# Kernel tuning notes

Hardware: AMD Instinct MI355X
Metric: run time of the kernel (lower is better)

Reference implementation:

```python
import jax, jax.numpy as jnp
import numpy as np

MAX_ITER = 10
EPS = 1e-4


def setup_inputs() -> dict:
    key = jax.random.key(0)
    k1, k2, k3 = jax.random.split(key, 3)
    B, N, M = 64, 1024, 1024
    s = jax.random.uniform(k1, (B, N, M), dtype=jnp.float32)
    nrows = jax.random.randint(k2, (B,), 0, N, dtype=jnp.int64 if jax.config.read('jax_enable_x64') else jnp.int32)
    ncols = jax.random.randint(k3, (B,), 0, M, dtype=nrows.dtype)
    return {"s": s, "nrows": nrows, "ncols": ncols}


def _sinkhorn(s, nrows, ncols):
    # Faithful to torch Sinkhorn.forward with exp=False, dummy_row=False.
    # The torch code builds [B,N,N]/[B,M,M] block-of-ones matrices and matmuls;
    # mathematically this is a masked column-sum (even iters) / row-sum (odd iters)
    # over the valid nrows[b] x ncols[b] block, followed by division inside the
    # block and zeroing outside it.
    B, N, M = s.shape
    row_mask = jnp.arange(N)[None, :] < nrows[:, None]            # [B, N]
    col_mask = jnp.arange(M)[None, :] < ncols[:, None]            # [B, M]
    mask = row_mask[:, :, None] & col_mask[:, None, :]            # [B, N, M]

    out = s + EPS
    for i in range(MAX_ITER):
        if i % 2 == 0:
            # column sums over valid rows -> [B, 1, M]
            sm = jnp.sum(jnp.where(row_mask[:, :, None], out, 0.0), axis=1, keepdims=True)
        else:
            # row sums over valid cols -> [B, N, 1]
            sm = jnp.sum(jnp.where(col_mask[:, None, :], out, 0.0), axis=2, keepdims=True)
        sm = jnp.where(sm == 0, 1.0, sm)  # guard (only affects masked-out entries)
        out = jnp.where(mask, out / sm, 0.0)
    return out


def reference(s, nrows, ncols):
    return _sinkhorn(s, nrows, ncols)
```

## Files before the change

### kernel.cpp

```cpp
#include <hip/hip_runtime.h>
#include <hip/hip_fp16.h>

#define EPS 1e-4f
constexpr int N_DIM  = 1024;
constexpr int M_DIM  = 1024;
constexpr int BATCH  = 64;
constexpr int CH     = 16;
constexpr int NPHASE = 5;


__global__ void zero_cnt(unsigned int* cnt) {
    const int t = threadIdx.x;
    if (t < NPHASE * BATCH) cnt[t] = 0u;
}

__device__ __forceinline__ void bat_barrier(unsigned int* cnt, int idx,
                                            unsigned int nact) {
    __syncthreads();
    if (threadIdx.x == 0) {
        __threadfence();
        atomicAdd(&cnt[idx], 1u);
        while (__hip_atomic_load(&cnt[idx], __ATOMIC_ACQUIRE,
                                 __HIP_MEMORY_SCOPE_AGENT) < nact)
            __builtin_amdgcn_s_sleep(8);
    }
    __syncthreads();
    __threadfence();
}

__global__ __launch_bounds__(256, 4)
void sinkhorn_one(const float* __restrict__ s,
                  const int* __restrict__ nrows,
                  const int* __restrict__ ncols,
                  __half* __restrict__ h,
                  float* __restrict__ tp0,
                  float* __restrict__ tp1,
                  unsigned int* __restrict__ cnt,
                  float* __restrict__ out)
{
    const int b  = blockIdx.y;
    const int ch = blockIdx.x;
    const int R = nrows[b], C = ncols[b];
    const size_t base = (size_t)b * N_DIM * M_DIM;
    const int tid = threadIdx.x, lane = tid & 63, wv = tid >> 6;
    const float4 z4 = make_float4(0.f, 0.f, 0.f, 0.f);

    for (int n = R + ch; n < N_DIM; n += CH)
        *(float4*)(out + base + (size_t)n * M_DIM + tid * 4) = z4;

    if (R == 0) return;
    const int CR = (R + CH - 1) / CH;
    const unsigned int nact = (unsigned int)((R + CR - 1) / CR);
    if ((unsigned int)ch >= nact) return;
    const int n0 = ch * CR;
    const int rows = min(R - n0, CR);
    const bool hi = (C > 512);

    __shared__ float clds[M_DIM];
    __shared__ float tp_lds[4][M_DIM];

    {
        const int m = tid * 4;
        float4 acc = z4;
        if (m < C) {
            for (int nn = 0; nn < rows; ++nn) {
                const size_t off = base + (size_t)(n0 + nn) * M_DIM + m;
                float4 v = *(const float4*)(s + off);
                v.x += EPS;
                v.y = (m + 1 < C) ? v.y + EPS : 0.f;
                v.z = (m + 2 < C) ? v.z + EPS : 0.f;
                v.w = (m + 3 < C) ? v.w + EPS : 0.f;
                acc.x += v.x; acc.y += v.y; acc.z += v.z; acc.w += v.w;
                union { __half2 h2[2]; uint2 u2; } pk;
                pk.h2[0] = __floats2half2_rn(v.x, v.y);
                pk.h2[1] = __floats2half2_rn(v.z, v.w);
                *(uint2*)(h + off) = pk.u2;
            }
        } else if (m < 512 || hi) {
            const uint2 zz = make_uint2(0u, 0u);
            for (int nn = 0; nn < rows; ++nn)
                *(uint2*)(h + base + (size_t)(n0 + nn) * M_DIM + m) = zz;
        }
        *(float4*)(tp0 + (size_t)(ch * BATCH + b) * M_DIM + m) = acc;
    }
    bat_barrier(cnt, 0 * BATCH + b, nact);

    const float* tpIn  = tp0;
    float*       tpOut = tp1;
    float crlo[8], crhi[8];

    for (int step = 0; step < 4; ++step) {
        {
            const int m = tid * 4;
            if (m < 512 || hi) {
                float4 sum = z4;
                for (unsigned int cc = 0; cc < nact; ++cc) {
                    float4 p = *(const float4*)(tpIn + (size_t)(cc * BATCH + b) * M_DIM + m);
                    sum.x += p.x; sum.y += p.y; sum.z += p.z; sum.w += p.w;
                }
                float4 cv;
                cv.x = (sum.x == 0.f) ? 1.f : 1.f / sum.x;
                cv.y = (sum.y == 0.f) ? 1.f : 1.f / sum.y;
                cv.z = (sum.z == 0.f) ? 1.f : 1.f / sum.z;
                cv.w = (sum.w == 0.f) ? 1.f : 1.f / sum.w;
                *(float4*)&clds[m] = cv;
            }
        }
        __syncthreads();
        {
            float4 a  = *(const float4*)&clds[lane * 8];
            float4 bb = *(const float4*)&clds[lane * 8 + 4];
            crlo[0]=a.x; crlo[1]=a.y; crlo[2]=a.z; crlo[3]=a.w;
            crlo[4]=bb.x; crlo[5]=bb.y; crlo[6]=bb.z; crlo[7]=bb.w;
            if (hi) {
                float4 d = *(const float4*)&clds[512 + lane * 8];
                float4 e = *(const float4*)&clds[512 + lane * 8 + 4];
                crhi[0]=d.x; crhi[1]=d.y; crhi[2]=d.z; crhi[3]=d.w;
                crhi[4]=e.x; crhi[5]=e.y; crhi[6]=e.z; crhi[7]=e.w;
            }
        }

        float tplo[8] = {0,0,0,0,0,0,0,0};
        float tphi[8] = {0,0,0,0,0,0,0,0};

        for (int nn = wv; nn < rows; nn += 4) {
            const int n = n0 + nn;
            const __half* hrow = h + base + (size_t)n * M_DIM;
            uint4 rlo = *(const uint4*)(hrow + lane * 8);
            float flo[8], fhi[8];
            {
                const __half2* hp = (const __half2*)&rlo;
#pragma unroll
                for (int k = 0; k < 4; ++k) {
                    float2 f = __half22float2(hp[k]);
                    flo[2*k] = f.x; flo[2*k+1] = f.y;
                }
            }
            float dot = 0.f;
#pragma unroll
            for (int k = 0; k < 8; ++k) dot += flo[k] * crlo[k];
            if (hi) {
                uint4 rhi = *(const uint4*)(hrow + 512 + lane * 8);
                const __half2* hq = (const __half2*)&rhi;
#pragma unroll
                for (int k = 0; k < 4; ++k) {
                    float2 f = __half22float2(hq[k]);
                    fhi[2*k] = f.x; fhi[2*k+1] = f.y;
                }
#pragma unroll
                for (int k = 0; k < 8; ++k) dot += fhi[k] * crhi[k];
            }
#pragma unroll
            for (int off = 32; off; off >>= 1) dot += __shfl_xor(dot, off);
            const float r = (dot == 0.f) ? 1.f : 1.f / dot;
#pragma unroll
            for (int k = 0; k < 8; ++k) tplo[k] += flo[k] * r;
            if (hi) {
#pragma unroll
                for (int k = 0; k < 8; ++k) tphi[k] += fhi[k] * r;
            }
        }

#pragma unroll
        for (int k = 0; k < 8; ++k) tp_lds[wv][lane * 8 + k] = tplo[k];
        if (hi) {
#pragma unroll
            for (int k = 0; k < 8; ++k) tp_lds[wv][512 + lane * 8 + k] = tphi[k];
        }
        __syncthreads();
        {
            const int m = tid * 4;
            if (m < 512 || hi) {
                float4 s0 = *(const float4*)&tp_lds[0][m];
                float4 s1 = *(const float4*)&tp_lds[1][m];
                float4 s2 = *(const float4*)&tp_lds[2][m];
                float4 s3 = *(const float4*)&tp_lds[3][m];
                *(float4*)(tpOut + (size_t)(ch * BATCH + b) * M_DIM + m) =
                    make_float4(s0.x+s1.x+s2.x+s3.x, s0.y+s1.y+s2.y+s3.y,
                                s0.z+s1.z+s2.z+s3.z, s0.w+s1.w+s2.w+s3.w);
            }
        }
        bat_barrier(cnt, (1 + step) * BATCH + b, nact);
        const float* ti = tpOut; tpOut = (float*)tpIn; tpIn = ti;
    }

    {
        const int m = tid * 4;
        if (m < 512 || hi) {
            float4 sum = z4;
            for (unsigned int cc = 0; cc < nact; ++cc) {
                float4 p = *(const float4*)(tpIn + (size_t)(cc * BATCH + b) * M_DIM + m);
                sum.x += p.x; sum.y += p.y; sum.z += p.z; sum.w += p.w;
            }
            float4 cv;
            cv.x = (sum.x == 0.f) ? 1.f : 1.f / sum.x;
            cv.y = (sum.y == 0.f) ? 1.f : 1.f / sum.y;
            cv.z = (sum.z == 0.f) ? 1.f : 1.f / sum.z;
            cv.w = (sum.w == 0.f) ? 1.f : 1.f / sum.w;
            *(float4*)&clds[m] = cv;
        }
    }
    __syncthreads();
    {
        float4 a  = *(const float4*)&clds[lane * 8];
        float4 bb = *(const float4*)&clds[lane * 8 + 4];
        crlo[0]=a.x; crlo[1]=a.y; crlo[2]=a.z; crlo[3]=a.w;
        crlo[4]=bb.x; crlo[5]=bb.y; crlo[6]=bb.z; crlo[7]=bb.w;
        if (hi) {
            float4 d = *(const float4*)&clds[512 + lane * 8];
            float4 e = *(const float4*)&clds[512 + lane * 8 + 4];
            crhi[0]=d.x; crhi[1]=d.y; crhi[2]=d.z; crhi[3]=d.w;
            crhi[4]=e.x; crhi[5]=e.y; crhi[6]=e.z; crhi[7]=e.w;
        }
    }
    for (int nn = wv; nn < rows; nn += 4) {
        const int n = n0 + nn;
        float* orow = out + base + (size_t)n * M_DIM;
        const __half* hrow = h + base + (size_t)n * M_DIM;
        uint4 rlo = *(const uint4*)(hrow + lane * 8);
        float flo[8], fhi[8];
        {
            const __half2* hp = (const __half2*)&rlo;
#pragma unroll
            for (int k = 0; k < 4; ++k) {
                float2 f = __half22float2(hp[k]);
                flo[2*k] = f.x; flo[2*k+1] = f.y;
            }
        }
        float dot = 0.f;
#pragma unroll
        for (int k = 0; k < 8; ++k) dot += flo[k] * crlo[k];
        if (hi) {
            uint4 rhi = *(const uint4*)(hrow + 512 + lane * 8);
            const __half2* hq = (const __half2*)&rhi;
#pragma unroll
            for (int k = 0; k < 4; ++k) {
                float2 f = __half22float2(hq[k]);
                fhi[2*k] = f.x; fhi[2*k+1] = f.y;
            }
#pragma unroll
            for (int k = 0; k < 8; ++k) dot += fhi[k] * crhi[k];
        }
#pragma unroll
        for (int off = 32; off; off >>= 1) dot += __shfl_xor(dot, off);
        const float r = (dot == 0.f) ? 1.f : 1.f / dot;

        *(float4*)(orow + lane * 8)     = make_float4(flo[0]*r*crlo[0], flo[1]*r*crlo[1],
                                                      flo[2]*r*crlo[2], flo[3]*r*crlo[3]);
        *(float4*)(orow + lane * 8 + 4) = make_float4(flo[4]*r*crlo[4], flo[5]*r*crlo[5],
                                                      flo[6]*r*crlo[6], flo[7]*r*crlo[7]);
        float4 o2 = z4, o3 = z4;
        if (hi) {
            o2 = make_float4(fhi[0]*r*crhi[0], fhi[1]*r*crhi[1],
                             fhi[2]*r*crhi[2], fhi[3]*r*crhi[3]);
            o3 = make_float4(fhi[4]*r*crhi[4], fhi[5]*r*crhi[5],
                             fhi[6]*r*crhi[6], fhi[7]*r*crhi[7]);
        }
        *(float4*)(orow + 512 + lane * 8)     = o2;
        *(float4*)(orow + 512 + lane * 8 + 4) = o3;
    }
}

constexpr int FCROWS = N_DIM / CH;

__global__ __launch_bounds__(256)
void conv_col0(const float* __restrict__ s, const int* __restrict__ nrows,
               const int* __restrict__ ncols, __half* __restrict__ h,
               float* __restrict__ tp0) {
    const int b  = blockIdx.y;
    const int mt = blockIdx.x & 3;
    const int ch = blockIdx.x >> 2;
    const int R = nrows[b], C = ncols[b];
    const int n0 = ch * FCROWS;
    if (n0 >= R) return;
    const int lane = threadIdx.x & 63, wv = threadIdx.x >> 6;
    const int m = mt * 256 + lane * 4;
    const int nend = min(R, n0 + FCROWS);
    const size_t base = (size_t)b * N_DIM * M_DIM;

    float4 acc = make_float4(0.f, 0.f, 0.f, 0.f);
    if (mt * 256 < C) {
        for (int n = n0 + wv; n < nend; n += 4) {
            float4 v = *(const float4*)(s + base + (size_t)n * M_DIM + m);
            v.x = (m + 0 < C) ? v.x + EPS : 0.f;
            v.y = (m + 1 < C) ? v.y + EPS : 0.f;
            v.z = (m + 2 < C) ? v.z + EPS : 0.f;
            v.w = (m + 3 < C) ? v.w + EPS : 0.f;
            acc.x += v.x; acc.y += v.y; acc.z += v.z; acc.w += v.w;
            union { __half2 h2[2]; uint2 u2; } pk;
            pk.h2[0] = __floats2half2_rn(v.x, v.y);
            pk.h2[1] = __floats2half2_rn(v.z, v.w);
            *(uint2*)(h + base + (size_t)n * M_DIM + m) = pk.u2;
        }
    } else {
        const uint2 z = make_uint2(0u, 0u);
        for (int n = n0 + wv; n < nend; n += 4)
            *(uint2*)(h + base + (size_t)n * M_DIM + m) = z;
    }
    __shared__ float4 red[4][64];
    red[wv][lane] = acc;
    __syncthreads();
    if (wv == 0) {
        float4 a0 = red[0][lane], a1 = red[1][lane],
               a2 = red[2][lane], a3 = red[3][lane];
        *(float4*)(tp0 + (size_t)(ch * BATCH + b) * M_DIM + m) =
            make_float4(a0.x+a1.x+a2.x+a3.x, a0.y+a1.y+a2.y+a3.y,
                        a0.z+a1.z+a2.z+a3.z, a0.w+a1.w+a2.w+a3.w);
    }
}

template <bool FINAL>
__global__ __launch_bounds__(256)
void row_step(const __half* __restrict__ h, const int* __restrict__ nrows,
              const int* __restrict__ ncols, const float* __restrict__ tpIn,
              float* __restrict__ tpOut, float* __restrict__ out) {
    const int b  = blockIdx.y;
    const int ch = blockIdx.x;
    const int R = nrows[b], C = ncols[b];
    const int n0 = ch * FCROWS;
    if (!FINAL && n0 >= R) return;
    const int lane = threadIdx.x & 63, wv = threadIdx.x >> 6;
    const size_t base = (size_t)b * N_DIM * M_DIM;
    const bool hi = (C > 512);
    const bool anyrows = (n0 < R);

    __shared__ float clds[M_DIM];
    __shared__ float tp_lds[4][M_DIM];

    float crlo[8], crhi[8];
    if (anyrows) {
        const int nch = min(CH, (R + FCROWS - 1) / FCROWS);
        const int t4 = threadIdx.x * 4;
        if (hi || t4 < 512) {
            float4 sum = make_float4(0.f, 0.f, 0.f, 0.f);
            for (int cc = 0; cc < nch; ++cc) {
                float4 p = *(const float4*)(tpIn + (size_t)(cc * BATCH + b) * M_DIM + t4);
                sum.x += p.x; sum.y += p.y; sum.z += p.z; sum.w += p.w;
            }
            float4 cv;
            cv.x = (sum.x == 0.f) ? 1.f : 1.f / sum.x;
            cv.y = (sum.y == 0.f) ? 1.f : 1.f / sum.y;
            cv.z = (sum.z == 0.f) ? 1.f : 1.f / sum.z;
            cv.w = (sum.w == 0.f) ? 1.f : 1.f / sum.w;
            *(float4*)&clds[t4] = cv;
        }
        __syncthreads();
        float4 a = *(const float4*)&clds[lane * 8];
        float4 bb = *(const float4*)&clds[lane * 8 + 4];
        crlo[0]=a.x; crlo[1]=a.y; crlo[2]=a.z; crlo[3]=a.w;
        crlo[4]=bb.x; crlo[5]=bb.y; crlo[6]=bb.z; crlo[7]=bb.w;
        if (hi) {
            float4 d = *(const float4*)&clds[512 + lane * 8];
            float4 e = *(const float4*)&clds[512 + lane * 8 + 4];
            crhi[0]=d.x; crhi[1]=d.y; crhi[2]=d.z; crhi[3]=d.w;
            crhi[4]=e.x; crhi[5]=e.y; crhi[6]=e.z; crhi[7]=e.w;
        }
    }

    float tplo[8] = {0,0,0,0,0,0,0,0};
    float tphi[8] = {0,0,0,0,0,0,0,0};

    for (int i = 0; i < 16; ++i) {
        const int n = n0 + wv * 16 + i;
        if (n < R) {
            const __half* hrow = h + base + (size_t)n * M_DIM;
            uint4 rlo = *(const uint4*)(hrow + lane * 8);
            float flo[8], fhi[8];
            const __half2* hp = (const __half2*)&rlo;
#pragma unroll
            for (int k = 0; k < 4; ++k) {
                float2 f = __half22float2(hp[k]);
                flo[2*k] = f.x; flo[2*k+1] = f.y;
            }
            float dot = 0.f;
#pragma unroll
            for (int k = 0; k < 8; ++k) dot += flo[k] * crlo[k];
            if (hi) {
                uint4 rhi = *(const uint4*)(hrow + 512 + lane * 8);
                const __half2* hq = (const __half2*)&rhi;
#pragma unroll
                for (int k = 0; k < 4; ++k) {
                    float2 f = __half22float2(hq[k]);
                    fhi[2*k] = f.x; fhi[2*k+1] = f.y;
                }
#pragma unroll
                for (int k = 0; k < 8; ++k) dot += fhi[k] * crhi[k];
            }
#pragma unroll
            for (int off = 32; off; off >>= 1) dot += __shfl_xor(dot, off);
            const float r = (dot == 0.f) ? 1.f : 1.f / dot;

            if (FINAL) {
                float* orow = out + base + (size_t)n * M_DIM;
                *(float4*)(orow + lane * 8)     = make_float4(flo[0]*r*crlo[0], flo[1]*r*crlo[1],
                                                              flo[2]*r*crlo[2], flo[3]*r*crlo[3]);
                *(float4*)(orow + lane * 8 + 4) = make_float4(flo[4]*r*crlo[4], flo[5]*r*crlo[5],
                                                              flo[6]*r*crlo[6], flo[7]*r*crlo[7]);
                float4 o2 = make_float4(0.f,0.f,0.f,0.f), o3 = o2;
                if (hi) {
                    o2 = make_float4(fhi[0]*r*crhi[0], fhi[1]*r*crhi[1],
                                     fhi[2]*r*crhi[2], fhi[3]*r*crhi[3]);
                    o3 = make_float4(fhi[4]*r*crhi[4], fhi[5]*r*crhi[5],
                                     fhi[6]*r*crhi[6], fhi[7]*r*crhi[7]);
                }
                *(float4*)(orow + 512 + lane * 8)     = o2;
                *(float4*)(orow + 512 + lane * 8 + 4) = o3;
            } else {
#pragma unroll
                for (int k = 0; k < 8; ++k) tplo[k] += flo[k] * r;
                if (hi) {
#pragma unroll
                    for (int k = 0; k < 8; ++k) tphi[k] += fhi[k] * r;
                }
            }
        } else if (FINAL) {
            float* orow = out + base + (size_t)n * M_DIM;
            const float4 z = make_float4(0.f, 0.f, 0.f, 0.f);
            *(float4*)(orow + lane * 8)           = z;
            *(float4*)(orow + lane * 8 + 4)       = z;
            *(float4*)(orow + 512 + lane * 8)     = z;
            *(float4*)(orow + 512 + lane * 8 + 4) = z;
        }
    }

    if (!FINAL) {
#pragma unroll
        for (int k = 0; k < 8; ++k) tp_lds[wv][lane * 8 + k] = tplo[k];
        if (hi) {
#pragma unroll
            for (int k = 0; k < 8; ++k) tp_lds[wv][512 + lane * 8 + k] = tphi[k];
        }
        __syncthreads();
        const int t4 = threadIdx.x * 4;
        if (hi || t4 < 512) {
            float4 s0 = *(const float4*)&tp_lds[0][t4];
            float4 s1 = *(const float4*)&tp_lds[1][t4];
            float4 s2 = *(const float4*)&tp_lds[2][t4];
            float4 s3 = *(const float4*)&tp_lds[3][t4];
            *(float4*)(tpOut + (size_t)(ch * BATCH + b) * M_DIM + t4) =
                make_float4(s0.x+s1.x+s2.x+s3.x, s0.y+s1.y+s2.y+s3.y,
                            s0.z+s1.z+s2.z+s3.z, s0.w+s1.w+s2.w+s3.w);
        }
    }
}

extern "C" void kernel_launch(void* const* d_in, const int* in_sizes, int n_in,
                              void* d_out, int out_size, void* d_ws, size_t ws_size,
                              hipStream_t stream) {
    const float* s     = (const float*)d_in[0];
    const int*   nrows = (const int*)d_in[1];
    const int*   ncols = (const int*)d_in[2];
    float*       out   = (float*)d_out;

    const size_t hElems  = (size_t)BATCH * N_DIM * M_DIM;
    const size_t tpElems = (size_t)CH * BATCH * M_DIM;
    const size_t need    = hElems * 2 + 2 * tpElems * 4 + NPHASE * BATCH * 4;

    if (ws_size >= need) {
        __half* h   = (__half*)d_ws;
        float*  tp0 = (float*)(h + hElems);
        float*  tp1 = tp0 + tpElems;
        unsigned int* cnt = (unsigned int*)(tp1 + tpElems);

        int dev = 0, numCU = 0, perCU = 0;
        hipGetDevice(&dev);
        hipDeviceGetAttribute(&numCU, hipDeviceAttributeMultiprocessorCount, dev);
        hipOccupancyMaxActiveBlocksPerMultiprocessor(&perCU, sinkhorn_one, 256, 0);

        if ((long long)perCU * numCU >= CH * BATCH) {
            zero_cnt<<<1, 320, 0, stream>>>(cnt);
            void* args[] = {(void*)&s, (void*)&nrows, (void*)&ncols, (void*)&h,
                            (void*)&tp0, (void*)&tp1, (void*)&cnt, (void*)&out};
            hipLaunchCooperativeKernel((void*)sinkhorn_one, dim3(CH, BATCH),
                                       dim3(256), args, 0, stream);
            return;
        }

        dim3 convGrid(4 * CH, BATCH), kGrid(CH, BATCH);
        conv_col0<<<convGrid, 256, 0, stream>>>(s, nrows, ncols, h, tp0);
        row_step<false><<<kGrid, 256, 0, stream>>>(h, nrows, ncols, tp0, tp1, out);
        row_step<false><<<kGrid, 256, 0, stream>>>(h, nrows, ncols, tp1, tp0, out);
        row_step<false><<<kGrid, 256, 0, stream>>>(h, nrows, ncols, tp0, tp1, out);
        row_step<false><<<kGrid, 256, 0, stream>>>(h, nrows, ncols, tp1, tp0, out);
        row_step<true ><<<kGrid, 256, 0, stream>>>(h, nrows, ncols, tp0, tp1, out);
        return;
    }
}
```

Measured before the change: 210.7 us.

## Distribute blocks across batches proportionally to valid rows; store partial sums as fp16

```diff
diff --git a/kernel.cpp b/kernel.cpp
--- a/kernel.cpp
+++ b/kernel.cpp
@@ -5,8 +5,10 @@
 constexpr int N_DIM  = 1024;
 constexpr int M_DIM  = 1024;
 constexpr int BATCH  = 64;
+constexpr int NB     = 1024;
+constexpr int NPHASE = 5;
+constexpr int WPAD   = 256;
 constexpr int CH     = 16;
-constexpr int NPHASE = 5;
 
 
 __global__ void zero_cnt(unsigned int* cnt) {
@@ -28,33 +30,63 @@
     __threadfence();
 }
 
+__device__ __forceinline__ void tp_store(__half* tp, size_t idx, float4 v) {
+    union { __half2 h2[2]; uint2 u; } pk;
+    pk.h2[0] = __floats2half2_rn(v.x, v.y);
+    pk.h2[1] = __floats2half2_rn(v.z, v.w);
+    *(uint2*)(tp + idx) = pk.u;
+}
+
 __global__ __launch_bounds__(256, 4)
-void sinkhorn_one(const float* __restrict__ s,
-                  const int* __restrict__ nrows,
-                  const int* __restrict__ ncols,
-                  __half* __restrict__ h,
-                  float* __restrict__ tp0,
-                  float* __restrict__ tp1,
-                  unsigned int* __restrict__ cnt,
-                  float* __restrict__ out)
+void sinkhorn_prop(const float* __restrict__ s,
+                   const int* __restrict__ nrows,
+                   const int* __restrict__ ncols,
+                   __half* __restrict__ h,
+                   __half* __restrict__ tp0,
+                   __half* __restrict__ tp1,
+                   unsigned int* __restrict__ cnt,
+                   float* __restrict__ out)
 {
-    const int b  = blockIdx.y;
-    const int ch = blockIdx.x;
-    const int R = nrows[b], C = ncols[b];
+    const int tid = threadIdx.x, lane = tid & 63, wv = tid >> 6;
+    __shared__ int sR[BATCH];
+    __shared__ int sNb[BATCH];
+    __shared__ int sPfx[BATCH + 1];
+
+    if (tid < BATCH) sR[tid] = nrows[tid];
+    __syncthreads();
+    if (tid == 0) {
+        long tot = 0;
+        for (int i = 0; i < BATCH; ++i) tot += sR[i] + WPAD;
+        int acc = 0;
+        for (int i = 0; i < BATCH; ++i) {
+            int nb = 1 + (int)(((long)(NB - BATCH) * (sR[i] + WPAD)) / tot);
+            sNb[i] = nb; sPfx[i] = acc; acc += nb;
+        }
+        sPfx[BATCH] = acc;
+    }
+    __syncthreads();
+
+    const int g = blockIdx.x;
+    if (g >= sPfx[BATCH]) return;
+    int b = BATCH - 1;
+    for (int i = 0; i < BATCH; ++i) { if (g < sPfx[i + 1]) { b = i; break; } }
+    const int l   = g - sPfx[b];
+    const int nbb = sNb[b];
+    const int R = sR[b], C = ncols[b];
     const size_t base = (size_t)b * N_DIM * M_DIM;
-    const int tid = threadIdx.x, lane = tid & 63, wv = tid >> 6;
     const float4 z4 = make_float4(0.f, 0.f, 0.f, 0.f);
 
-    for (int n = R + ch; n < N_DIM; n += CH)
+    for (int n = R + l; n < N_DIM; n += nbb)
         *(float4*)(out + base + (size_t)n * M_DIM + tid * 4) = z4;
-
     if (R == 0) return;
-    const int CR = (R + CH - 1) / CH;
+
+    const int CR = (R + nbb - 1) / nbb;
     const unsigned int nact = (unsigned int)((R + CR - 1) / CR);
-    if ((unsigned int)ch >= nact) return;
-    const int n0 = ch * CR;
+    if ((unsigned int)l >= nact) return;
+    const int n0 = l * CR;
     const int rows = min(R - n0, CR);
     const bool hi = (C > 512);
+    const int g0 = sPfx[b];
 
     __shared__ float clds[M_DIM];
     __shared__ float tp_lds[4][M_DIM];
@@ -81,12 +113,13 @@
             for (int nn = 0; nn < rows; ++nn)
                 *(uint2*)(h + base + (size_t)(n0 + nn) * M_DIM + m) = zz;
         }
-        *(float4*)(tp0 + (size_t)(ch * BATCH + b) * M_DIM + m) = acc;
+        if (m < 512 || hi)
+            tp_store(tp0, (size_t)g * M_DIM + m, acc);
     }
     bat_barrier(cnt, 0 * BATCH + b, nact);
 
-    const float* tpIn  = tp0;
-    float*       tpOut = tp1;
+    const __half* tpIn  = tp0;
+    __half*       tpOut = tp1;
     float crlo[8], crhi[8];
 
     for (int step = 0; step < 4; ++step) {
@@ -95,8 +128,11 @@
             if (m < 512 || hi) {
                 float4 sum = z4;
                 for (unsigned int cc = 0; cc < nact; ++cc) {
-                    float4 p = *(const float4*)(tpIn + (size_t)(cc * BATCH + b) * M_DIM + m);
-                    sum.x += p.x; sum.y += p.y; sum.z += p.z; sum.w += p.w;
+                    uint2 raw = *(const uint2*)(tpIn + (size_t)(g0 + cc) * M_DIM + m);
+                    const __half2* hp = (const __half2*)&raw;
+                    float2 f0 = __half22float2(hp[0]);
+                    float2 f1 = __half22float2(hp[1]);
+                    sum.x += f0.x; sum.y += f0.y; sum.z += f1.x; sum.w += f1.y;
                 }
                 float4 cv;
                 cv.x = (sum.x == 0.f) ? 1.f : 1.f / sum.x;
@@ -124,8 +160,7 @@
         float tphi[8] = {0,0,0,0,0,0,0,0};
 
         for (int nn = wv; nn < rows; nn += 4) {
-            const int n = n0 + nn;
-            const __half* hrow = h + base + (size_t)n * M_DIM;
+            const __half* hrow = h + base + (size_t)(n0 + nn) * M_DIM;
             uint4 rlo = *(const uint4*)(hrow + lane * 8);
             float flo[8], fhi[8];
             {
@@ -175,13 +210,13 @@
                 float4 s1 = *(const float4*)&tp_lds[1][m];
                 float4 s2 = *(const float4*)&tp_lds[2][m];
                 float4 s3 = *(const float4*)&tp_lds[3][m];
-                *(float4*)(tpOut + (size_t)(ch * BATCH + b) * M_DIM + m) =
-                    make_float4(s0.x+s1.x+s2.x+s3.x, s0.y+s1.y+s2.y+s3.y,
-                                s0.z+s1.z+s2.z+s3.z, s0.w+s1.w+s2.w+s3.w);
+                tp_store(tpOut, (size_t)g * M_DIM + m,
+                         make_float4(s0.x+s1.x+s2.x+s3.x, s0.y+s1.y+s2.y+s3.y,
+                                     s0.z+s1.z+s2.z+s3.z, s0.w+s1.w+s2.w+s3.w));
             }
         }
         bat_barrier(cnt, (1 + step) * BATCH + b, nact);
-        const float* ti = tpOut; tpOut = (float*)tpIn; tpIn = ti;
+        const __half* ti = tpOut; tpOut = (__half*)tpIn; tpIn = ti;
     }
 
     {
@@ -189,8 +224,11 @@
         if (m < 512 || hi) {
             float4 sum = z4;
             for (unsigned int cc = 0; cc < nact; ++cc) {
-                float4 p = *(const float4*)(tpIn + (size_t)(cc * BATCH + b) * M_DIM + m);
-                sum.x += p.x; sum.y += p.y; sum.z += p.z; sum.w += p.w;
+                uint2 raw = *(const uint2*)(tpIn + (size_t)(g0 + cc) * M_DIM + m);
+                const __half2* hp = (const __half2*)&raw;
+                float2 f0 = __half22float2(hp[0]);
+                float2 f1 = __half22float2(hp[1]);
+                sum.x += f0.x; sum.y += f0.y; sum.z += f1.x; sum.w += f1.y;
             }
             float4 cv;
             cv.x = (sum.x == 0.f) ? 1.f : 1.f / sum.x;
@@ -213,6 +251,7 @@
             crhi[4]=e.x; crhi[5]=e.y; crhi[6]=e.z; crhi[7]=e.w;
         }
     }
+    const float4 z0 = make_float4(0.f, 0.f, 0.f, 0.f);
     for (int nn = wv; nn < rows; nn += 4) {
         const int n = n0 + nn;
         float* orow = out + base + (size_t)n * M_DIM;
@@ -249,7 +288,7 @@
                                                       flo[2]*r*crlo[2], flo[3]*r*crlo[3]);
         *(float4*)(orow + lane * 8 + 4) = make_float4(flo[4]*r*crlo[4], flo[5]*r*crlo[5],
                                                       flo[6]*r*crlo[6], flo[7]*r*crlo[7]);
-        float4 o2 = z4, o3 = z4;
+        float4 o2 = z0, o3 = z0;
         if (hi) {
             o2 = make_float4(fhi[0]*r*crhi[0], fhi[1]*r*crhi[1],
                              fhi[2]*r*crhi[2], fhi[3]*r*crhi[3]);
@@ -452,37 +491,40 @@
     const int*   ncols = (const int*)d_in[2];
     float*       out   = (float*)d_out;
 
-    const size_t hElems  = (size_t)BATCH * N_DIM * M_DIM;
-    const size_t tpElems = (size_t)CH * BATCH * M_DIM;
-    const size_t need    = hElems * 2 + 2 * tpElems * 4 + NPHASE * BATCH * 4;
+    const size_t hElems   = (size_t)BATCH * N_DIM * M_DIM;
+    const size_t tpRegion = (size_t)16 * 1024 * 1024;
+    const size_t need     = hElems * 2 + tpRegion + NPHASE * BATCH * 4;
 
     if (ws_size >= need) {
-        __half* h   = (__half*)d_ws;
-        float*  tp0 = (float*)(h + hElems);
-        float*  tp1 = tp0 + tpElems;
-        unsigned int* cnt = (unsigned int*)(tp1 + tpElems);
+        __half* h    = (__half*)d_ws;
+        char*   tpRg = (char*)(h + hElems);
+        unsigned int* cnt = (unsigned int*)(tpRg + tpRegion);
 
         int dev = 0, numCU = 0, perCU = 0;
         hipGetDevice(&dev);
         hipDeviceGetAttribute(&numCU, hipDeviceAttributeMultiprocessorCount, dev);
-        hipOccupancyMaxActiveBlocksPerMultiprocessor(&perCU, sinkhorn_one, 256, 0);
-
-        if ((long long)perCU * numCU >= CH * BATCH) {
+        hipOccupancyMaxActiveBlocksPerMultiprocessor(&perCU, sinkhorn_prop, 256, 0);
+
+        if ((long long)perCU * numCU >= NB) {
+            __half* tp0 = (__half*)tpRg;
+            __half* tp1 = tp0 + (size_t)NB * M_DIM;
             zero_cnt<<<1, 320, 0, stream>>>(cnt);
             void* args[] = {(void*)&s, (void*)&nrows, (void*)&ncols, (void*)&h,
                             (void*)&tp0, (void*)&tp1, (void*)&cnt, (void*)&out};
-            hipLaunchCooperativeKernel((void*)sinkhorn_one, dim3(CH, BATCH),
+            hipLaunchCooperativeKernel((void*)sinkhorn_prop, dim3(NB),
                                        dim3(256), args, 0, stream);
             return;
         }
 
+        float* tp0f = (float*)tpRg;
+        float* tp1f = tp0f + (size_t)CH * BATCH * M_DIM;
         dim3 convGrid(4 * CH, BATCH), kGrid(CH, BATCH);
-        conv_col0<<<convGrid, 256, 0, stream>>>(s, nrows, ncols, h, tp0);
-        row_step<false><<<kGrid, 256, 0, stream>>>(h, nrows, ncols, tp0, tp1, out);
-        row_step<false><<<kGrid, 256, 0, stream>>>(h, nrows, ncols, tp1, tp0, out);
-        row_step<false><<<kGrid, 256, 0, stream>>>(h, nrows, ncols, tp0, tp1, out);
-        row_step<false><<<kGrid, 256, 0, stream>>>(h, nrows, ncols, tp1, tp0, out);
-        row_step<true ><<<kGrid, 256, 0, stream>>>(h, nrows, ncols, tp0, tp1, out);
+        conv_col0<<<convGrid, 256, 0, stream>>>(s, nrows, ncols, h, tp0f);
+        row_step<false><<<kGrid, 256, 0, stream>>>(h, nrows, ncols, tp0f, tp1f, out);
+        row_step<false><<<kGrid, 256, 0, stream>>>(h, nrows, ncols, tp1f, tp0f, out);
+        row_step<false><<<kGrid, 256, 0, stream>>>(h, nrows, ncols, tp0f, tp1f, out);
+        row_step<false><<<kGrid, 256, 0, stream>>>(h, nrows, ncols, tp1f, tp0f, out);
+        row_step<true ><<<kGrid, 256, 0, stream>>>(h, nrows, ncols, tp0f, tp1f, out);
         return;
     }
 }
```

New measurement: 206.2 us. 2.1% less time.
